# Optimization experiments

Measured on AMD Instinct MI355X. Metric: run time of the kernel, lower is better.

Reference implementation:

```python
import jax, jax.numpy as jnp
import numpy as np

N_HEADS = 16
D_QKV = 128
THETA = 10000.0


def setup_inputs() -> dict:
    key = jax.random.key(0)
    k1, k2, k3 = jax.random.split(key, 3)
    B, L, d_model = 2, 2048, 2048
    X = jax.random.normal(k1, (B, L, d_model), jnp.float32)
    # torch Linear weight is (out,in); we store the transposed (in,out) layout so y = X @ W
    W_qkv = jax.random.normal(k2, (d_model, 3 * N_HEADS * D_QKV), jnp.float32) / np.sqrt(d_model)
    W_out = jax.random.normal(k3, (N_HEADS * D_QKV, d_model), jnp.float32) / np.sqrt(N_HEADS * D_QKV)
    return {"X": X, "W_qkv": W_qkv, "W_out": W_out}


def _rope(x, cos, sin):
    # interleaved-pair RoPE (rotary-embedding-torch style): pairs are (x[2i], x[2i+1])
    x1 = x[..., 0::2]
    x2 = x[..., 1::2]
    out = jnp.stack([x1 * cos - x2 * sin, x1 * sin + x2 * cos], axis=-1)
    return out.reshape(x.shape)


def reference(X, W_qkv, W_out):
    B, L, _ = X.shape
    H, D = N_HEADS, D_QKV
    # fused QKV projection; layout per head is [q|k|v] of size 3*D (matches 'b l (h ddd)')
    qkv = (X @ W_qkv).reshape(B, L, H, 3 * D).transpose(0, 2, 1, 3)  # b h l 3d
    Q, K, V = jnp.split(qkv, 3, axis=-1)                              # each b h l d
    inv_freq = 1.0 / (THETA ** (jnp.arange(0, D, 2, dtype=jnp.float32) / D))
    ang = jnp.arange(L, dtype=jnp.float32)[:, None] * inv_freq[None, :]  # (L, D/2)
    cos, sin = jnp.cos(ang), jnp.sin(ang)
    Q = _rope(Q, cos, sin)
    K = _rope(K, cos, sin)
    # causal SDPA
    scores = jnp.einsum('bhqd,bhkd->bhqk', Q, K) / jnp.sqrt(jnp.float32(D))
    causal = jnp.tril(jnp.ones((L, L), dtype=bool))
    scores = jnp.where(causal, scores, -jnp.inf)
    attn = jax.nn.softmax(scores, axis=-1)
    out = jnp.einsum('bhqk,bhkd->bqhd', attn, V).reshape(B, L, H * D)
    return out @ W_out
```

## Files before the change

### kernel.cpp

```cpp
#include <hip/hip_runtime.h>

typedef __bf16 bf16x8 __attribute__((ext_vector_type(8)));
typedef float f32x4 __attribute__((ext_vector_type(4)));
typedef float f32x16 __attribute__((ext_vector_type(16)));
typedef unsigned u32x4 __attribute__((ext_vector_type(4)));

#define LSEQ 2048

__device__ __forceinline__ unsigned short f2b(float f){
  unsigned u = __builtin_bit_cast(unsigned, f);
  u += 0x7FFFu + ((u >> 16) & 1u);
  return (unsigned short)(u >> 16);
}
__device__ __forceinline__ float b2f(unsigned short h){
  unsigned u = ((unsigned)h) << 16;
  return __builtin_bit_cast(float, u);
}
__device__ __forceinline__ unsigned cvt_pk_bf16(float lo, float hi){
  unsigned r;
  asm("v_cvt_pk_bf16_f32 %0, %1, %2" : "=v"(r) : "v"(lo), "v"(hi));
  return r;
}

typedef __attribute__((address_space(1))) const unsigned int glb_u32;
typedef __attribute__((address_space(3))) unsigned int lds_u32;
__device__ __forceinline__ void gld_lds16(const void* g, void* l){
  __builtin_amdgcn_global_load_lds((glb_u32*)g, (lds_u32*)l, 16, 0, 0);
}

__global__ __launch_bounds__(256) void cvt_f32_bf16(const float* __restrict__ in,
                                                    unsigned short* __restrict__ out){
  int tid = blockIdx.x * 256 + threadIdx.x;
  float4 v = reinterpret_cast<const float4*>(in)[tid];
  ushort4 o;
  o.x = f2b(v.x); o.y = f2b(v.y); o.z = f2b(v.z); o.w = f2b(v.w);
  reinterpret_cast<ushort4*>(out)[tid] = o;
}

__global__ __launch_bounds__(256) void transpose_cvt(const float* __restrict__ in,
                                                     unsigned short* __restrict__ out,
                                                     int R, int C){
  __shared__ float t[32][33];
  int c0 = blockIdx.x * 32, r0 = blockIdx.y * 32;
  int tx = threadIdx.x, ty = threadIdx.y;
  #pragma unroll
  for (int i = 0; i < 4; i++){
    int r = ty + i*8;
    t[r][tx] = in[(size_t)(r0 + r) * C + c0 + tx];
  }
  __syncthreads();
  #pragma unroll
  for (int i = 0; i < 4; i++){
    int c = ty + i*8;
    out[(size_t)(c0 + c) * R + r0 + tx] = f2b(t[tx][c]);
  }
}

__global__ __launch_bounds__(256) void trig_init(float* __restrict__ cosT,
                                                 float* __restrict__ sinT){
  int tid = blockIdx.x * 256 + threadIdx.x;
  int i = tid & 63; int l = tid >> 6;
  float invf = powf(10000.0f, -((float)(2*i)) / 128.0f);
  float ang = (float)l * invf;
  cosT[tid] = cosf(ang);
  sinT[tid] = sinf(ang);
}

__global__ __launch_bounds__(256) void rope_qk(const unsigned short* __restrict__ qkv,
                                               const float* __restrict__ cosT,
                                               const float* __restrict__ sinT,
                                               unsigned short* __restrict__ Qr,
                                               unsigned short* __restrict__ Kr){
  int tid = blockIdx.x * 256 + threadIdx.x;
  int i  = tid & 63;
  int l  = (tid >> 6) & (LSEQ - 1);
  int bh = tid >> 17;
  int b = bh >> 4, h = bh & 15;
  size_t base = (size_t)(b*LSEQ + l) * 6144 + h*384;
  float c = cosT[l*64 + i], s = sinT[l*64 + i];
  float q1 = b2f(qkv[base + 2*i]),       q2 = b2f(qkv[base + 2*i + 1]);
  float k1 = b2f(qkv[base + 128 + 2*i]), k2 = b2f(qkv[base + 128 + 2*i + 1]);
  const float qs = 0.12751691f;
  size_t ob = ((size_t)bh*LSEQ + l) * 128;
  Qr[ob + 2*i]     = f2b((q1*c - q2*s) * qs);
  Qr[ob + 2*i + 1] = f2b((q1*s + q2*c) * qs);
  Kr[ob + 2*i]     = f2b(k1*c - k2*s);
  Kr[ob + 2*i + 1] = f2b(k1*s + k2*c);
}

__global__ __launch_bounds__(256) void vtrans(const unsigned short* __restrict__ qkv,
                                              unsigned short* __restrict__ Vt){
  __shared__ unsigned short t[64][65];
  int d0 = blockIdx.x * 64, l0 = blockIdx.y * 64, bh = blockIdx.z;
  int b = bh >> 4, h = bh & 15;
  int tx = threadIdx.x, ty = threadIdx.y;
  #pragma unroll
  for (int i = 0; i < 16; i++){
    int lr = ty + i*4;
    t[lr][tx] = qkv[(size_t)(b*LSEQ + l0 + lr) * 6144 + h*384 + 256 + d0 + tx];
  }
  __syncthreads();
  #pragma unroll
  for (int i = 0; i < 16; i++){
    int dr = ty + i*4;
    Vt[(size_t)(bh*128 + d0 + dr) * LSEQ + l0 + tx] = t[tx][dr];
  }
}

template<bool BF16_OUT>
__global__ __launch_bounds__(256) void gemm_bt(const unsigned short* __restrict__ A,
                                               const unsigned short* __restrict__ Bt,
                                               void* __restrict__ Cp,
                                               int M, int N, int K){
  __shared__ __align__(16) unsigned short As[128*64];
  __shared__ __align__(16) unsigned short Bs[128*64];
  int m0 = blockIdx.y * 128, n0 = blockIdx.x * 128;
  int tid = threadIdx.x, lane = tid & 63, wave = tid >> 6;
  int wm = wave >> 1, wn = wave & 1;
  int lr = lane & 15, lh = lane >> 4;
  int r8 = lane >> 3;
  int cg = (lane & 7) ^ r8;
  f32x4 acc[4][4];
  #pragma unroll
  for (int a = 0; a < 4; a++)
    #pragma unroll
    for (int bb = 0; bb < 4; bb++)
      acc[a][bb] = (f32x4){0.f, 0.f, 0.f, 0.f};

  const unsigned short* Abase = A  + (size_t)(m0 + wave*32 + r8)*K + cg*8;
  const unsigned short* Bbase = Bt + (size_t)(n0 + wave*32 + r8)*K + cg*8;

  int nk = K >> 6;
  for (int k0 = 0; k0 < nk; k0++){
    __syncthreads();
    #pragma unroll
    for (int i = 0; i < 4; i++){
      gld_lds16(Abase + (size_t)i*8*K + k0*64, &As[(wave*32 + i*8)*64]);
      gld_lds16(Bbase + (size_t)i*8*K + k0*64, &Bs[(wave*32 + i*8)*64]);
    }
    __syncthreads();
    #pragma unroll
    for (int kk = 0; kk < 2; kk++){
      bf16x8 af[4], bfg[4];
      #pragma unroll
      for (int f = 0; f < 4; f++){
        int ra = wm*64 + f*16 + lr;
        af[f]  = *reinterpret_cast<const bf16x8*>(&As[ra*64 + (((kk*4 + lh) ^ (ra & 7)) * 8)]);
        int rb = wn*64 + f*16 + lr;
        bfg[f] = *reinterpret_cast<const bf16x8*>(&Bs[rb*64 + (((kk*4 + lh) ^ (rb & 7)) * 8)]);
      }
      __builtin_amdgcn_s_setprio(1);
      #pragma unroll
      for (int fm = 0; fm < 4; fm++)
        #pragma unroll
        for (int fn = 0; fn < 4; fn++)
          acc[fm][fn] = __builtin_amdgcn_mfma_f32_16x16x32_bf16(af[fm], bfg[fn], acc[fm][fn], 0, 0, 0);
      __builtin_amdgcn_s_setprio(0);
    }
  }
  #pragma unroll
  for (int fm = 0; fm < 4; fm++)
    #pragma unroll
    for (int fn = 0; fn < 4; fn++)
      #pragma unroll
      for (int r = 0; r < 4; r++){
        int row = m0 + wm*64 + fm*16 + lh*4 + r;
        int col = n0 + wn*64 + fn*16 + lr;
        float v = acc[fm][fn][r];
        if (BF16_OUT) ((unsigned short*)Cp)[(size_t)row*N + col] = f2b(v);
        else          ((float*)Cp)[(size_t)row*N + col] = v;
      }
}

__global__ __launch_bounds__(256, 2) void attn_kernel(const unsigned short* __restrict__ Qr,
                                                      const unsigned short* __restrict__ Kr,
                                                      const unsigned short* __restrict__ Vt,
                                                      unsigned short* __restrict__ aout){
  __shared__ __align__(16) unsigned short Ks[2][64*128];
  __shared__ __align__(16) unsigned short Vs[2][128*64];
  int bh = blockIdx.x;
  int y = blockIdx.y;
  int qi = (y < 8) ? (15 - y) : (y - 8);
  int q0 = qi * 128;
  int tid = threadIdx.x;
  int wave = tid >> 6, lane = tid & 63;
  int ql = lane & 31;
  int hi = lane >> 5;
  int b = bh >> 4, h = bh & 15;

  bf16x8 qf[8];
  const unsigned short* Qb = Qr + ((size_t)bh*LSEQ + q0 + wave*32 + ql) * 128 + hi*8;
  #pragma unroll
  for (int ks = 0; ks < 8; ks++)
    qf[ks] = *reinterpret_cast<const bf16x8*>(Qb + ks*16);

  float m_i = -1.0e38f, l_i = 0.f;
  f32x16 o[4];
  #pragma unroll
  for (int nd = 0; nd < 4; nd++) o[nd] = (f32x16)(0.f);

  const unsigned short* Kbh = Kr + (size_t)bh*LSEQ*128;
  const unsigned short* Vbh = Vt + (size_t)bh*128*LSEQ;
  int klrow = lane >> 4;
  int vlrow = lane >> 3;
  int vg = (lane & 7) ^ vlrow;

  int ntiles = (q0 >> 6) + 2;

  #pragma unroll
  for (int i = 0; i < 4; i++){
    int rk = wave*16 + i*4 + klrow;
    int gk = (lane & 15) ^ (rk & 7);
    gld_lds16(Kbh + (size_t)rk*128 + gk*8, &Ks[0][(wave*16 + i*4)*128]);
    int rv = wave*32 + i*8 + vlrow;
    gld_lds16(Vbh + (size_t)rv*LSEQ + vg*8, &Vs[0][(wave*32 + i*8)*64]);
  }
  __syncthreads();

  int cur = 0;
  for (int t = 0; t < ntiles; t++){
    if (t + 1 < ntiles){
      int kv1 = (t + 1) * 64;
      #pragma unroll
      for (int i = 0; i < 4; i++){
        int rk = wave*16 + i*4 + klrow;
        int gk = (lane & 15) ^ (rk & 7);
        gld_lds16(Kbh + (size_t)(kv1 + rk)*128 + gk*8, &Ks[cur^1][(wave*16 + i*4)*128]);
        int rv = wave*32 + i*8 + vlrow;
        gld_lds16(Vbh + (size_t)rv*LSEQ + kv1 + vg*8, &Vs[cur^1][(wave*32 + i*8)*64]);
      }
    }
    int kv0 = t * 64;

    f32x16 sa0 = (f32x16)(0.f), sa1 = (f32x16)(0.f);
    __builtin_amdgcn_s_setprio(1);
    #pragma unroll
    for (int ks = 0; ks < 8; ks++){
      int g = 2*ks + hi;
      bf16x8 kf0 = *reinterpret_cast<const bf16x8*>(&Ks[cur][ql*128 + ((g ^ (ql & 7)) * 8)]);
      bf16x8 kf1 = *reinterpret_cast<const bf16x8*>(&Ks[cur][(32 + ql)*128 + ((g ^ ((32 + ql) & 7)) * 8)]);
      sa0 = __builtin_amdgcn_mfma_f32_32x32x16_bf16(kf0, qf[ks], sa0, 0, 0, 0);
      sa1 = __builtin_amdgcn_mfma_f32_32x32x16_bf16(kf1, qf[ks], sa1, 0, 0, 0);
    }
    __builtin_amdgcn_s_setprio(0);

    if (t >= ntiles - 2){
      int q = q0 + wave*32 + ql;
      #pragma unroll
      for (int r = 0; r < 16; r++){
        int kvb = kv0 + (r & 3) + 8*(r >> 2) + 4*hi;
        if (kvb > q)      sa0[r] = -1.0e38f;
        if (kvb + 32 > q) sa1[r] = -1.0e38f;
      }
    }

    float pm = -1.0e38f;
    #pragma unroll
    for (int r = 0; r < 16; r++) pm = fmaxf(pm, fmaxf(sa0[r], sa1[r]));
    pm = fmaxf(pm, __shfl_xor(pm, 32, 64));

    if (__any(pm > m_i + 8.0f)){
      float mn = fmaxf(m_i, pm);
      float al = exp2f(m_i - mn);
      m_i = mn;
      l_i *= al;
      #pragma unroll
      for (int r = 0; r < 16; r++){
        int qsrc = (r & 3) + 8*(r >> 2) + 4*hi;
        float alr = __shfl(al, qsrc, 64);
        o[0][r] *= alr; o[1][r] *= alr; o[2][r] *= alr; o[3][r] *= alr;
      }
    }

    float ps = 0.f;
    unsigned wlo[2][4], whi[2][4];
    #pragma unroll
    for (int a = 0; a < 4; a++){
      float p0 = exp2f(sa0[4*a]     - m_i);
      float p1 = exp2f(sa0[4*a + 1] - m_i);
      float p2 = exp2f(sa0[4*a + 2] - m_i);
      float p3 = exp2f(sa0[4*a + 3] - m_i);
      ps += (p0 + p1) + (p2 + p3);
      wlo[0][a] = cvt_pk_bf16(p0, p1);
      whi[0][a] = cvt_pk_bf16(p2, p3);
      float p4 = exp2f(sa1[4*a]     - m_i);
      float p5 = exp2f(sa1[4*a + 1] - m_i);
      float p6 = exp2f(sa1[4*a + 2] - m_i);
      float p7 = exp2f(sa1[4*a + 3] - m_i);
      ps += (p4 + p5) + (p6 + p7);
      wlo[1][a] = cvt_pk_bf16(p4, p5);
      whi[1][a] = cvt_pk_bf16(p6, p7);
    }
    ps += __shfl_xor(ps, 32, 64);
    l_i += ps;

    bf16x8 pa[4];
    #pragma unroll
    for (int h2 = 0; h2 < 2; h2++)
      #pragma unroll
      for (int a0 = 0; a0 < 4; a0 += 2){
        unsigned x  = wlo[h2][a0], y  = wlo[h2][a0 + 1];
        asm("v_permlane32_swap_b32 %0, %1" : "+v"(x), "+v"(y));
        unsigned x2 = whi[h2][a0], y2 = whi[h2][a0 + 1];
        asm("v_permlane32_swap_b32 %0, %1" : "+v"(x2), "+v"(y2));
        u32x4 w4 = (u32x4){x, x2, y, y2};
        pa[2*h2 + (a0 >> 1)] = __builtin_bit_cast(bf16x8, w4);
      }

    __builtin_amdgcn_s_setprio(1);
    #pragma unroll
    for (int ks = 0; ks < 4; ks++){
      int g = 2*ks + hi;
      #pragma unroll
      for (int nd = 0; nd < 4; nd++){
        int dr = nd*32 + ql;
        bf16x8 vf = *reinterpret_cast<const bf16x8*>(&Vs[cur][dr*64 + ((g ^ (dr & 7)) * 8)]);
        o[nd] = __builtin_amdgcn_mfma_f32_32x32x16_bf16(pa[ks], vf, o[nd], 0, 0, 0);
      }
    }
    __builtin_amdgcn_s_setprio(0);

    __syncthreads();
    cur ^= 1;
  }

  float inv = 1.0f / l_i;
  #pragma unroll
  for (int r = 0; r < 16; r++){
    int qsrc = (r & 3) + 8*(r >> 2) + 4*hi;
    float invr = __shfl(inv, qsrc, 64);
    int q = q0 + wave*32 + qsrc;
    size_t rowb = ((size_t)b*LSEQ + q)*2048 + h*128 + ql;
    aout[rowb]      = f2b(o[0][r] * invr);
    aout[rowb + 32] = f2b(o[1][r] * invr);
    aout[rowb + 64] = f2b(o[2][r] * invr);
    aout[rowb + 96] = f2b(o[3][r] * invr);
  }
}

extern "C" void kernel_launch(void* const* d_in, const int* in_sizes, int n_in,
                              void* d_out, int out_size, void* d_ws, size_t ws_size,
                              hipStream_t stream){
  const float* X  = (const float*)d_in[0];
  const float* Wq = (const float*)d_in[1];
  const float* Wo = (const float*)d_in[2];
  float* out = (float*)d_out;
  char* ws = (char*)d_ws;
  unsigned short* Xb   = (unsigned short*)(ws + 0);
  unsigned short* Wt   = (unsigned short*)(ws + 16777216);
  unsigned short* Wot  = (unsigned short*)(ws + 41943040);
  unsigned short* QKV  = (unsigned short*)(ws + 50331648);
  unsigned short* Kr   = (unsigned short*)(ws + 100663296);
  unsigned short* Vt   = (unsigned short*)(ws + 117440512);
  float* cosT          = (float*)(ws + 134217728);
  float* sinT          = (float*)(ws + 134742016);
  unsigned short* Qr   = Xb;
  unsigned short* Aout = QKV;

  cvt_f32_bf16<<<8192, 256, 0, stream>>>(X, Xb);
  transpose_cvt<<<dim3(192, 64), dim3(32, 8), 0, stream>>>(Wq, Wt, 2048, 6144);
  transpose_cvt<<<dim3(64, 64),  dim3(32, 8), 0, stream>>>(Wo, Wot, 2048, 2048);
  trig_init<<<512, 256, 0, stream>>>(cosT, sinT);
  gemm_bt<true><<<dim3(48, 32), 256, 0, stream>>>(Xb, Wt, (void*)QKV, 4096, 6144, 2048);
  rope_qk<<<16384, 256, 0, stream>>>(QKV, cosT, sinT, Qr, Kr);
  vtrans<<<dim3(2, 32, 32), dim3(64, 4), 0, stream>>>(QKV, Vt);
  attn_kernel<<<dim3(32, 16), 256, 0, stream>>>(Qr, Kr, Vt, Aout);
  gemm_bt<false><<<dim3(16, 32), 256, 0, stream>>>(Aout, Wot, (void*)out, 4096, 2048, 2048);
}
```

Before: 380.8 us.

## Pipeline GEMM K-loop with four-stage LDS ring and async prefetch

Replaces the GEMM's single-buffered K=64 tile loop, which synchronized twice per step, with a four-stage LDS ring of K=32 tiles. Loads are issued three stages ahead and the loop waits with a vmcnt count and one barrier per iteration. It also changes the LDS XOR swizzle to suit the narrower tile and adds an occupancy hint of two blocks per CU. The aim is to hide global-to-LDS load latency behind MFMA work, at the cost of more LDS use and tighter synchronization (the vmcnt(8) count must match the loads in flight).

After: 387.7 us. About the same (+1.8%).

```diff
diff --git a/kernel.cpp b/kernel.cpp
--- a/kernel.cpp
+++ b/kernel.cpp
@@ -108,18 +108,16 @@
 }
 
 template<bool BF16_OUT>
-__global__ __launch_bounds__(256) void gemm_bt(const unsigned short* __restrict__ A,
-                                               const unsigned short* __restrict__ Bt,
-                                               void* __restrict__ Cp,
-                                               int M, int N, int K){
-  __shared__ __align__(16) unsigned short As[128*64];
-  __shared__ __align__(16) unsigned short Bs[128*64];
+__global__ __launch_bounds__(256, 2) void gemm_p4(const unsigned short* __restrict__ A,
+                                                  const unsigned short* __restrict__ Bt,
+                                                  void* __restrict__ Cp,
+                                                  int M, int N, int K){
+  __shared__ __align__(16) unsigned short Ls[4][2][4096];
   int m0 = blockIdx.y * 128, n0 = blockIdx.x * 128;
   int tid = threadIdx.x, lane = tid & 63, wave = tid >> 6;
   int wm = wave >> 1, wn = wave & 1;
   int lr = lane & 15, lh = lane >> 4;
-  int r8 = lane >> 3;
-  int cg = (lane & 7) ^ r8;
+
   f32x4 acc[4][4];
   #pragma unroll
   for (int a = 0; a < 4; a++)
@@ -127,37 +125,55 @@
     for (int bb = 0; bb < 4; bb++)
       acc[a][bb] = (f32x4){0.f, 0.f, 0.f, 0.f};
 
-  const unsigned short* Abase = A  + (size_t)(m0 + wave*32 + r8)*K + cg*8;
-  const unsigned short* Bbase = Bt + (size_t)(n0 + wave*32 + r8)*K + cg*8;
-
-  int nk = K >> 6;
-  for (int k0 = 0; k0 < nk; k0++){
-    __syncthreads();
-    #pragma unroll
-    for (int i = 0; i < 4; i++){
-      gld_lds16(Abase + (size_t)i*8*K + k0*64, &As[(wave*32 + i*8)*64]);
-      gld_lds16(Bbase + (size_t)i*8*K + k0*64, &Bs[(wave*32 + i*8)*64]);
-    }
-    __syncthreads();
-    #pragma unroll
-    for (int kk = 0; kk < 2; kk++){
-      bf16x8 af[4], bfg[4];
-      #pragma unroll
-      for (int f = 0; f < 4; f++){
-        int ra = wm*64 + f*16 + lr;
-        af[f]  = *reinterpret_cast<const bf16x8*>(&As[ra*64 + (((kk*4 + lh) ^ (ra & 7)) * 8)]);
-        int rb = wn*64 + f*16 + lr;
-        bfg[f] = *reinterpret_cast<const bf16x8*>(&Bs[rb*64 + (((kk*4 + lh) ^ (rb & 7)) * 8)]);
-      }
-      __builtin_amdgcn_s_setprio(1);
-      #pragma unroll
-      for (int fm = 0; fm < 4; fm++)
-        #pragma unroll
-        for (int fn = 0; fn < 4; fn++)
-          acc[fm][fn] = __builtin_amdgcn_mfma_f32_16x16x32_bf16(af[fm], bfg[fn], acc[fm][fn], 0, 0, 0);
-      __builtin_amdgcn_s_setprio(0);
-    }
-  }
+  int g0 = tid, g1 = tid + 256;
+  int ra0 = g0 >> 2, kg0 = (g0 & 3) ^ ((ra0 >> 1) & 3);
+  int ra1 = g1 >> 2, kg1 = (g1 & 3) ^ ((ra1 >> 1) & 3);
+  const unsigned short* As0 = A  + (size_t)(m0 + ra0)*K + kg0*8;
+  const unsigned short* As1 = A  + (size_t)(m0 + ra1)*K + kg1*8;
+  const unsigned short* Bs0 = Bt + (size_t)(n0 + ra0)*K + kg0*8;
+  const unsigned short* Bs1 = Bt + (size_t)(n0 + ra1)*K + kg1*8;
+  int d0 = wave*512, d1 = 2048 + wave*512;
+
+  int sl = (lh ^ ((lr >> 1) & 3)) * 8;
+
+  int nk = K >> 5;
+
+  #define STAGE(kt, s) do { \
+    gld_lds16(As0 + (size_t)(kt)*32, &Ls[s][0][d0]); \
+    gld_lds16(As1 + (size_t)(kt)*32, &Ls[s][0][d1]); \
+    gld_lds16(Bs0 + (size_t)(kt)*32, &Ls[s][1][d0]); \
+    gld_lds16(Bs1 + (size_t)(kt)*32, &Ls[s][1][d1]); \
+  } while (0)
+
+  STAGE(0, 0);
+  STAGE(1, 1);
+  STAGE(2, 2);
+
+  #pragma unroll 1
+  for (int t = 0; t < nk; t++){
+    int s = t & 3;
+    asm volatile("s_waitcnt vmcnt(8)" ::: "memory");
+    __builtin_amdgcn_s_barrier();
+    __builtin_amdgcn_sched_barrier(0);
+    if (t + 3 < nk) STAGE(t + 3, (t + 3) & 3);
+    bf16x8 af[4], bfr[4];
+    #pragma unroll
+    for (int f = 0; f < 4; f++){
+      int ra = wm*64 + f*16 + lr;
+      af[f]  = *reinterpret_cast<const bf16x8*>(&Ls[s][0][ra*32 + sl]);
+      int rb = wn*64 + f*16 + lr;
+      bfr[f] = *reinterpret_cast<const bf16x8*>(&Ls[s][1][rb*32 + sl]);
+    }
+    __builtin_amdgcn_s_setprio(1);
+    #pragma unroll
+    for (int fm = 0; fm < 4; fm++)
+      #pragma unroll
+      for (int fn = 0; fn < 4; fn++)
+        acc[fm][fn] = __builtin_amdgcn_mfma_f32_16x16x32_bf16(af[fm], bfr[fn], acc[fm][fn], 0, 0, 0);
+    __builtin_amdgcn_s_setprio(0);
+  }
+  #undef STAGE
+
   #pragma unroll
   for (int fm = 0; fm < 4; fm++)
     #pragma unroll
@@ -361,9 +377,9 @@
   transpose_cvt<<<dim3(192, 64), dim3(32, 8), 0, stream>>>(Wq, Wt, 2048, 6144);
   transpose_cvt<<<dim3(64, 64),  dim3(32, 8), 0, stream>>>(Wo, Wot, 2048, 2048);
   trig_init<<<512, 256, 0, stream>>>(cosT, sinT);
-  gemm_bt<true><<<dim3(48, 32), 256, 0, stream>>>(Xb, Wt, (void*)QKV, 4096, 6144, 2048);
+  gemm_p4<true><<<dim3(48, 32), 256, 0, stream>>>(Xb, Wt, (void*)QKV, 4096, 6144, 2048);
   rope_qk<<<16384, 256, 0, stream>>>(QKV, cosT, sinT, Qr, Kr);
   vtrans<<<dim3(2, 32, 32), dim3(64, 4), 0, stream>>>(QKV, Vt);
   attn_kernel<<<dim3(32, 16), 256, 0, stream>>>(Qr, Kr, Vt, Aout);
-  gemm_bt<false><<<dim3(16, 32), 256, 0, stream>>>(Aout, Wot, (void*)out, 4096, 2048, 2048);
-}
+  gemm_p4<false><<<dim3(16, 32), 256, 0, stream>>>(Aout, Wot, (void*)out, 4096, 2048, 2048);
+}
```
